# Performance work log

Hardware: AMD Instinct MI355X
Metric: run time of the kernel (lower is better)

The kernel has to match this reference:

```python
import jax, jax.numpy as jnp
import numpy as np

B, TQ, TKV, NPR, H, D = 4, 1024, 1024, 5, 16, 64
IN, OUT, R, P, NT = 1024, H * D, 64, 4096, 4
KV = NPR + TKV  # prompt tokens prepended to kv sequence


def setup_inputs() -> dict:
    key = jax.random.key(0)
    ks = jax.random.split(key, 20)
    n = lambda k, shp, s: jax.random.normal(k, shp, jnp.float32) * s
    W = 0.02  # weight init scale
    return {
        "pe": n(ks[0], (P, OUT), 1.0),
        "attn_output": n(ks[1], (B, TQ, OUT), 1.0),
        "q": n(ks[2], (B, H, TQ, D), 1.0),
        "kv_query": n(ks[3], (B, TKV, IN), 1.0),
        "attn_mask": jnp.zeros((TQ, KV), jnp.float32),
        "prompt": n(ks[4], (NT, NPR, IN), 1.0),
        "gates": n(ks[5], (1,), 1.0),
        "k_w1": n(ks[6], (IN, R), W), "k_w2": n(ks[7], (R, OUT), W),
        "v_w1": n(ks[8], (IN, R), W), "v_w2": n(ks[9], (R, OUT), W),
        "kp_w1": n(ks[10], (OUT, R), W), "kp_w2": n(ks[11], (R, OUT), W),
        "qp_w1": n(ks[12], (OUT, R), W), "qp_w2": n(ks[13], (R, OUT), W),
        "indices_a": jax.random.randint(ks[14], (B, TQ), 0, P),
        "indices_b": jax.random.randint(ks[15], (B, TKV), 0, P),
        "task_idx": jax.random.randint(ks[16], (B,), 0, NT),
    }


def reference(pe, attn_output, q, kv_query, attn_mask, prompt, gates,
              k_w1, k_w2, v_w1, v_w2, kp_w1, kp_w2, qp_w1, qp_w2,
              indices_a, indices_b, task_idx):
    # prompt selection + concat in front of kv sequence
    pr = prompt[task_idx]                                   # [B, NPR, IN]
    kv_x = jnp.concatenate([pr, kv_query], axis=1)          # [B, KV, IN]
    # positional features; key_pos is zero-padded over the prompt slots
    key_pos = jnp.pad(pe[indices_b], ((0, 0), (NPR, 0), (0, 0)))  # [B, KV, OUT]
    # low-rank projections
    k = (kv_x @ k_w1) @ k_w2 + (key_pos @ kp_w1) @ kp_w2    # [B, KV, OUT]
    v = (kv_x @ v_w1) @ v_w2                                # [B, KV, OUT]
    q_pos = (pe[indices_a] @ qp_w1) @ qp_w2                 # [B, TQ, OUT]
    qh = q + q_pos.reshape(B, TQ, H, D).transpose(0, 2, 1, 3)
    kh = k.reshape(B, KV, H, D).transpose(0, 2, 1, 3)
    vh = v.reshape(B, KV, H, D).transpose(0, 2, 1, 3)
    scores = jnp.einsum('bhqd,bhkd->bhqk', qh, kh) / np.float32(np.sqrt(D))
    scores = scores + attn_mask[None, None]                 # 2D mask path
    w = jax.nn.softmax(scores, axis=-1)                     # dropout = identity (eval)
    out = jnp.einsum('bhqk,bhkd->bhqd', w, vh)
    out = out.transpose(0, 2, 1, 3).reshape(B, TQ, OUT)
    return out * gates + attn_output
```

## Files before the change

kernel.cpp:

```cpp
#include <hip/hip_runtime.h>
#include <hip/hip_bf16.h>

#define B_    4
#define TQ_   1024
#define TKV_  1024
#define NPR_  5
#define H_    16
#define D_    64
#define IN_   1024
#define OUT_  1024
#define R_    64
#define KV_   1029
#define KVP_  1088
#define M1_   4116
#define M1P_  4160
#define MQ_   4096
#define NKT_  17
#define NQT_  16
#define MR_   (M1P_ * R_)
#define LOG2E_ 1.4426950408889634f
#define SQ_SCALE_ (0.125f * 1.4426950408889634f)

typedef __attribute__((ext_vector_type(8))) short short8;
typedef __attribute__((ext_vector_type(4))) float f32x4;
typedef __attribute__((ext_vector_type(4))) unsigned uint4v;
typedef __attribute__((ext_vector_type(2))) unsigned uint2v;

#define MFMA(a, b, c) __builtin_amdgcn_mfma_f32_16x16x32_bf16(a, b, c, 0, 0, 0)

#define AS1 __attribute__((address_space(1)))
#define AS3 __attribute__((address_space(3)))
#define GLDS(g, l) __builtin_amdgcn_global_load_lds((const AS1 void*)(g), (AS3 void*)(l), 16, 0, 0)

static __device__ __forceinline__ short f2bf(float f) {
  unsigned u = __builtin_bit_cast(unsigned, f);
  u += 0x7fffu + ((u >> 16) & 1u);
  return (short)(u >> 16);
}
static __device__ __forceinline__ float bf2f(unsigned short u) {
  return __builtin_bit_cast(float, (unsigned)u << 16);
}
static __device__ __forceinline__ short8 zero8() {
  short8 z = {0, 0, 0, 0, 0, 0, 0, 0};
  return z;
}
static __device__ __forceinline__ unsigned cvtpk(float lo, float hi) {
  unsigned r;
  asm("v_cvt_pk_bf16_f32 %0, %1, %2" : "=v"(r) : "v"(lo), "v"(hi));
  return r;
}
static __device__ __forceinline__ float vexp2(float x) {
  float r;
  asm("v_exp_f32 %0, %1" : "=v"(r) : "v"(x));
  return r;
}
static __device__ __forceinline__ void pl32(unsigned &a, unsigned &b) {
  asm("v_permlane32_swap_b32 %0, %1" : "+v"(a), "+v"(b));
}
static __device__ __forceinline__ void pl16(unsigned &a, unsigned &b) {
  asm("v_permlane16_swap_b32 %0, %1" : "+v"(a), "+v"(b));
}
static __device__ __forceinline__ float redsum4(float x) {
  unsigned a = __builtin_bit_cast(unsigned, x), b = a;
  pl16(a, b);
  x = __builtin_bit_cast(float, a) + __builtin_bit_cast(float, b);
  a = b = __builtin_bit_cast(unsigned, x);
  pl32(a, b);
  return __builtin_bit_cast(float, a) + __builtin_bit_cast(float, b);
}
static __device__ __forceinline__ void cd2bfrag(const f32x4 (&s)[4], short8 &p0, short8 &p1) {
  unsigned u00 = cvtpk(s[0][0], s[0][1]), u01 = cvtpk(s[0][2], s[0][3]);
  unsigned u10 = cvtpk(s[1][0], s[1][1]), u11 = cvtpk(s[1][2], s[1][3]);
  unsigned u20 = cvtpk(s[2][0], s[2][1]), u21 = cvtpk(s[2][2], s[2][3]);
  unsigned u30 = cvtpk(s[3][0], s[3][1]), u31 = cvtpk(s[3][2], s[3][3]);
  pl32(u00, u10); pl32(u01, u11); pl32(u20, u30); pl32(u21, u31);
  pl16(u00, u10); pl16(u01, u11); pl16(u20, u30); pl16(u21, u31);
  uint4v w0 = {u00, u01, u10, u11};
  uint4v w1 = {u20, u21, u30, u31};
  p0 = __builtin_bit_cast(short8, w0);
  p1 = __builtin_bit_cast(short8, w1);
}
static __device__ __forceinline__ short8 sum4pack(const unsigned short* p) {
  f32x4 lo = {0, 0, 0, 0}, hi = {0, 0, 0, 0};
#pragma unroll
  for (int c = 0; c < 4; ++c) {
    short8 v = *(const short8*)(p + (size_t)c * MR_);
#pragma unroll
    for (int j = 0; j < 4; ++j) {
      lo[j] += bf2f((unsigned short)v[j]);
      hi[j] += bf2f((unsigned short)v[j + 4]);
    }
  }
  uint4v u = {cvtpk(lo[0], lo[1]), cvtpk(lo[2], lo[3]),
              cvtpk(hi[0], hi[1]), cvtpk(hi[2], hi[3])};
  return __builtin_bit_cast(short8, u);
}

__global__ __launch_bounds__(256) void prep(
    const float* __restrict__ kw1, const float* __restrict__ vw1,
    const float* __restrict__ kpw1, const float* __restrict__ qpw1,
    const float* __restrict__ kw2, const float* __restrict__ vw2,
    const float* __restrict__ kpw2, const float* __restrict__ qpw2,
    const float* __restrict__ mask, const float* __restrict__ pe,
    short* __restrict__ w1t, short* __restrict__ w2t,
    short* __restrict__ pebf, int* __restrict__ mflags) {
  int bid = blockIdx.x;
  if (bid < 64) {
    int tid = bid * 256 + threadIdx.x;
    const float* w1s[4] = {kw1, vw1, kpw1, qpw1};
    const float* w2s[4] = {kw2, vw2, kpw2, qpw2};
    for (int i = tid; i < 4 * R_ * IN_; i += 64 * 256) {
      int m = i >> 16, p = i & 65535, r = p >> 10, k = p & 1023;
      w1t[i] = f2bf(w1s[m][k * R_ + r]);
    }
    for (int i = tid; i < 4 * OUT_ * R_; i += 64 * 256) {
      int m = i >> 16, p = i & 65535, o = p >> 6, r = p & 63;
      w2t[i] = f2bf(w2s[m][r * OUT_ + o]);
    }
  } else if (bid < 336) {
    int t = bid - 64;
    int qt = t / NKT_, kt = t % NKT_;
    int nz = 0;
    for (int it = 0; it < 16; ++it) {
      int e = it * 256 + threadIdx.x;
      int rr = e >> 6, cc = e & 63;
      int kv = kt * 64 + cc;
      if (kv < KV_) {
        float v = mask[(size_t)(qt * 64 + rr) * KV_ + kv];
        nz |= (v != 0.0f);
      }
    }
    __shared__ int snz[4];
    unsigned long long bv = __ballot(nz);
    if ((threadIdx.x & 63) == 0) snz[threadIdx.x >> 6] = (bv != 0ULL);
    __syncthreads();
    if (threadIdx.x == 0) mflags[t] = snz[0] | snz[1] | snz[2] | snz[3];
  } else {
    int pb = bid - 336;
#pragma unroll
    for (int it = 0; it < 8; ++it) {
      int i = pb * 16384 + it * 2048 + threadIdx.x * 8;
      f32x4 a0 = *(const f32x4*)(pe + i);
      f32x4 a1 = *(const f32x4*)(pe + i + 4);
      uint4v u = {cvtpk(a0[0], a0[1]), cvtpk(a0[2], a0[3]),
                  cvtpk(a1[0], a1[1]), cvtpk(a1[2], a1[3])};
      *(uint4v*)(pebf + i) = u;
    }
  }
}

__global__ __launch_bounds__(256) void stage1(
    const float* __restrict__ prompt, const float* __restrict__ kv_query,
    const short* __restrict__ pebf, const int* __restrict__ indices_a,
    const int* __restrict__ indices_b, const int* __restrict__ task_idx,
    const short* __restrict__ w1t, unsigned short* __restrict__ part) {
  int which = blockIdx.z;
  int chunk = blockIdx.y;
  int mbase = blockIdx.x * 64;
  int lane = threadIdx.x & 63, wave = threadIdx.x >> 6;
  int lrow = lane & 15, lg = lane >> 4;
  int row = mbase + wave * 16 + lrow;

  const float* asrc_f = nullptr;
  const short* asrc_b = nullptr;
  if (which == 0) {
    int r = min(row, M1_ - 1);
    int b = r / KV_, t = r - b * KV_;
    asrc_f = (t < NPR_) ? prompt + (size_t)(task_idx[b] * NPR_ + t) * IN_
                        : kv_query + (size_t)(b * TKV_ + t - NPR_) * IN_;
  } else if (which == 1) {
    int r = min(row, M1_ - 1);
    int b = r / KV_, t = r - b * KV_;
    if (t >= NPR_) asrc_b = pebf + (size_t)indices_b[b * TKV_ + t - NPR_] * OUT_;
  } else {
    int r = min(row, MQ_ - 1);
    asrc_b = pebf + (size_t)indices_a[r] * OUT_;
  }
  const short* bt0 = w1t + (size_t)((which == 0) ? 0 : (which == 1) ? 2 : 3) * (R_ * IN_);
  const short* bt1 = w1t + (size_t)1 * (R_ * IN_);
  int k0base = chunk * 256;

  const f32x4 fz = {0, 0, 0, 0};
  f32x4 acc0[4], acc1[4];
#pragma unroll
  for (int f = 0; f < 4; ++f) { acc0[f] = fz; acc1[f] = fz; }

#pragma unroll
  for (int ks = 0; ks < 8; ++ks) {
    int kc = k0base + ks * 32 + lg * 8;
    short8 bdat;
    if (which == 0) {
      f32x4 a0 = *(const f32x4*)(asrc_f + kc);
      f32x4 a1 = *(const f32x4*)(asrc_f + kc + 4);
      uint4v au = {cvtpk(a0[0], a0[1]), cvtpk(a0[2], a0[3]),
                   cvtpk(a1[0], a1[1]), cvtpk(a1[2], a1[3])};
      bdat = __builtin_bit_cast(short8, au);
    } else {
      bdat = asrc_b ? *(const short8*)(asrc_b + kc) : zero8();
    }
#pragma unroll
    for (int f = 0; f < 4; ++f) {
      short8 w0 = *(const short8*)(bt0 + (size_t)(f * 16 + lrow) * IN_ + kc);
      acc0[f] = MFMA(w0, bdat, acc0[f]);
      if (which == 0) {
        short8 w1f = *(const short8*)(bt1 + (size_t)(f * 16 + lrow) * IN_ + kc);
        acc1[f] = MFMA(w1f, bdat, acc1[f]);
      }
    }
  }
  int o0 = (which == 0) ? 0 : (which == 1) ? 2 : 3;
  size_t mrow = (size_t)(mbase + wave * 16 + lrow) * R_;
  unsigned short* p0 = part + (size_t)(o0 * 4 + chunk) * MR_ + mrow;
#pragma unroll
  for (int f = 0; f < 4; ++f) {
    uint2v w = {cvtpk(acc0[f][0], acc0[f][1]), cvtpk(acc0[f][2], acc0[f][3])};
    *(uint2v*)(p0 + f * 16 + lg * 4) = w;
  }
  if (which == 0) {
    unsigned short* p1 = part + (size_t)(4 + chunk) * MR_ + mrow;
#pragma unroll
    for (int f = 0; f < 4; ++f) {
      uint2v w = {cvtpk(acc1[f][0], acc1[f][1]), cvtpk(acc1[f][2], acc1[f][3])};
      *(uint2v*)(p1 + f * 16 + lg * 4) = w;
    }
  }
}

__global__ __launch_bounds__(256) void stage2(
    const unsigned short* __restrict__ part, const short* __restrict__ w2t,
    short* __restrict__ kbf, short* __restrict__ vtb, short* __restrict__ tqs) {
  int L = blockIdx.x;
  int lane = threadIdx.x & 63, wave = threadIdx.x >> 6;
  int lrow = lane & 15, lg = lane >> 4;
  const f32x4 fz = {0, 0, 0, 0};

  if (L < 272) {
    int virt = (L & 7) * 34 + (L >> 3);
    int mt = virt >> 2, nh = virt & 3;
    int orow = mt * 64 + wave * 16 + lrow;
    int ob = orow / KVP_, okv = orow - ob * KVP_;
    bool valid = (okv < KV_);
    int kt = okv >> 6, rin = okv & 63;
    int prow = ob * KV_ + min(okv, KV_ - 1);
    short8 b1[2], b2[2];
#pragma unroll
    for (int ks = 0; ks < 2; ++ks) {
      int kc = ks * 32 + lg * 8;
      b1[ks] = valid ? sum4pack(part + (size_t)prow * R_ + kc) : zero8();
      b2[ks] = valid ? sum4pack(part + (size_t)8 * MR_ + (size_t)prow * R_ + kc) : zero8();
    }
    const short* w2k  = w2t;
    const short* w2kp = w2t + (size_t)2 * (OUT_ * R_);
    int sw = (rin & 7) << 3;
#pragma unroll
    for (int i = 0; i < 4; ++i) {
      int nbase = (nh * 4 + i) * 64;
      int h = nbase >> 6;
      f32x4 acc[4];
#pragma unroll
      for (int f = 0; f < 4; ++f) acc[f] = fz;
#pragma unroll
      for (int ks = 0; ks < 2; ++ks) {
        int kc = ks * 32 + lg * 8;
#pragma unroll
        for (int f = 0; f < 4; ++f) {
          short8 aK  = *(const short8*)(w2k  + (size_t)(nbase + f * 16 + lrow) * R_ + kc);
          short8 aKP = *(const short8*)(w2kp + (size_t)(nbase + f * 16 + lrow) * R_ + kc);
          acc[f] = MFMA(aK,  b1[ks], acc[f]);
          acc[f] = MFMA(aKP, b2[ks], acc[f]);
        }
      }
      size_t tb = ((size_t)((ob * H_ + h) * NKT_ + kt) << 12);
#pragma unroll
      for (int f = 0; f < 4; ++f) {
        float v0 = valid ? acc[f][0] : 0.f, v1 = valid ? acc[f][1] : 0.f;
        float v2 = valid ? acc[f][2] : 0.f, v3 = valid ? acc[f][3] : 0.f;
        uint2v w = {cvtpk(v0, v1), cvtpk(v2, v3)};
        int d0 = f * 16 + lg * 4;
        *(uint2v*)(kbf + tb + rin * 64 + (d0 ^ sw)) = w;
      }
    }
  } else if (L < 544) {
    int Lm = L - 272;
    int virt = (Lm & 7) * 34 + (Lm >> 3);
    int cb = virt >> 2, oh = virt & 3;
    short8 afr[8];
#pragma unroll
    for (int f = 0; f < 4; ++f)
#pragma unroll
      for (int ks = 0; ks < 2; ++ks) {
        int crow = cb * 64 + f * 16 + lrow;
        int bb = crow / KVP_, kvr = crow - bb * KVP_;
        afr[f * 2 + ks] = (kvr < KV_)
            ? sum4pack(part + (size_t)4 * MR_ + (size_t)(bb * KV_ + kvr) * R_ + ks * 32 + lg * 8)
            : zero8();
      }
    int bb = (cb * 64) / KVP_;
    int kvbase = cb * 64 - bb * KVP_;
    int kt = kvbase >> 6;
    const short* w2v = w2t + (size_t)1 * (OUT_ * R_);
#pragma unroll
    for (int i = 0; i < 4; ++i) {
      int obase = (oh * 4 + i) * 64;
      int o = obase + wave * 16 + lrow;
      int h = o >> 6, d = o & 63;
      f32x4 acc[4];
#pragma unroll
      for (int f = 0; f < 4; ++f) acc[f] = fz;
#pragma unroll
      for (int ks = 0; ks < 2; ++ks) {
        short8 bw = *(const short8*)(w2v + (size_t)o * R_ + ks * 32 + lg * 8);
#pragma unroll
        for (int f = 0; f < 4; ++f) acc[f] = MFMA(afr[f * 2 + ks], bw, acc[f]);
      }
      int sw = (d & 7) << 3;
      size_t tb = ((size_t)((bb * H_ + h) * NKT_ + kt) << 12);
#pragma unroll
      for (int f = 0; f < 4; ++f) {
        int kvin0 = f * 16 + lg * 4;
        float v0 = (kvbase + kvin0 + 0 < KV_) ? acc[f][0] : 0.f;
        float v1 = (kvbase + kvin0 + 1 < KV_) ? acc[f][1] : 0.f;
        float v2 = (kvbase + kvin0 + 2 < KV_) ? acc[f][2] : 0.f;
        float v3 = (kvbase + kvin0 + 3 < KV_) ? acc[f][3] : 0.f;
        uint2v w = {cvtpk(v0, v1), cvtpk(v2, v3)};
        *(uint2v*)(vtb + tb + d * 64 + (kvin0 ^ sw)) = w;
      }
    }
  } else {
    int j = L - 544;
#pragma unroll
    for (int it = 0; it < 8; ++it) {
      int idx = j * 16384 + it * 2048 + threadIdx.x * 8;
      short8 v = sum4pack(part + (size_t)12 * MR_ + idx);
      *(short8*)(tqs + idx) = v;
    }
  }
}

__global__ __launch_bounds__(256, 3) void attn(
    const short* __restrict__ tqs, const short* __restrict__ w2t,
    const float* __restrict__ qin,
    const short* __restrict__ kbf, const short* __restrict__ vtb,
    const float* __restrict__ mask, const int* __restrict__ mflags,
    const float* __restrict__ gates, const float* __restrict__ attn_in,
    float* __restrict__ out) {
  int bid = blockIdx.x;
  int xcd = bid & 7, wg = bid >> 3;
  int qt = wg & 15, g = wg >> 4;
  int grp = xcd * 8 + g;
  int h = grp & 15, b = grp >> 4;

  int lane = threadIdx.x & 63, wave = threadIdx.x >> 6;
  int lrow = lane & 15, lg = lane >> 4;
  int qbase = qt * 64 + wave * 16;

  __shared__ __align__(16) short kvls[3][2][4096];

  const short* ktile = kbf + ((size_t)grp * NKT_ << 12);
  const short* vtile = vtb + ((size_t)grp * NKT_ << 12);
  const short* kg = ktile + wave * 512 + lane * 8;
  const short* vg = vtile + wave * 512 + lane * 8;

  int sw = (lrow & 7) << 3;
  int offA = (lg * 8) ^ sw;
  int offB = (32 + lg * 8) ^ sw;
  const short* p0A = &kvls[0][0][lrow * 64 + offA];
  const short* p0B = &kvls[0][0][lrow * 64 + offB];
  const short* p1A = &kvls[1][0][lrow * 64 + offA];
  const short* p1B = &kvls[1][0][lrow * 64 + offB];
  const short* p2A = &kvls[2][0][lrow * 64 + offA];
  const short* p2B = &kvls[2][0][lrow * 64 + offB];
  const int* mfp = mflags + qt * NKT_;

  auto stage = [&](int t, int bsel) {
    const short* ks = kg + ((size_t)t << 12);
    const short* vs = vg + ((size_t)t << 12);
    GLDS(ks,        &kvls[bsel][0][wave * 512]);
    GLDS(ks + 2048, &kvls[bsel][0][wave * 512 + 2048]);
    GLDS(vs,        &kvls[bsel][1][wave * 512]);
    GLDS(vs + 2048, &kvls[bsel][1][wave * 512 + 2048]);
  };

  stage(0, 0);
  stage(1, 1);

  int fl = 0;
#pragma unroll
  for (int t = 0; t < NKT_; ++t) fl |= (mfp[t] ? 1 : 0) << t;
  fl = __builtin_amdgcn_readfirstlane(fl);

  const f32x4 fz = {0, 0, 0, 0};
  short8 qa0, qa1;
  {
    const short* w2q = w2t + (size_t)3 * (OUT_ * R_);
    f32x4 qs[4];
#pragma unroll
    for (int f = 0; f < 4; ++f) qs[f] = fz;
#pragma unroll
    for (int ks = 0; ks < 2; ++ks) {
      short8 tqf = *(const short8*)(tqs + (size_t)(b * TQ_ + qbase + lrow) * R_ + ks * 32 + lg * 8);
#pragma unroll
      for (int f = 0; f < 4; ++f) {
        short8 wf = *(const short8*)(w2q + (size_t)(h * 64 + f * 16 + lrow) * R_ + ks * 32 + lg * 8);
        qs[f] = MFMA(wf, tqf, qs[f]);
      }
    }
    const float* qrow = qin + (size_t)(b * TQ_ + qbase + lrow) * OUT_ + h * 64;
#pragma unroll
    for (int f = 0; f < 4; ++f) {
      f32x4 qv = *(const f32x4*)(qrow + f * 16 + lg * 4);
#pragma unroll
      for (int r = 0; r < 4; ++r) qs[f][r] = (qs[f][r] + qv[r]) * SQ_SCALE_;
    }
    cd2bfrag(qs, qa0, qa1);
  }

  f32x4 oacc[4];
#pragma unroll
  for (int f = 0; f < 4; ++f) oacc[f] = fz;
  float plsum = 0.f;

  auto tile = [&](int t, const short* pA, const short* pB, int sb, int mode) {
    if (mode == 2) asm volatile("s_waitcnt vmcnt(0)" ::: "memory");
    else           asm volatile("s_waitcnt vmcnt(4)" ::: "memory");
    __builtin_amdgcn_sched_barrier(0);
    __builtin_amdgcn_s_barrier();
    __builtin_amdgcn_sched_barrier(0);
    if (mode == 0) stage(t + 2, sb);

    f32x4 s[4];
#pragma unroll
    for (int f = 0; f < 4; ++f) {
      short8 kA = *(const short8*)(pA + f * 1024);
      short8 kB = *(const short8*)(pB + f * 1024);
      s[f] = MFMA(kA, qa0, fz);
      s[f] = MFMA(kB, qa1, s[f]);
    }
    short8 vfr[8];
#pragma unroll
    for (int f = 0; f < 4; ++f) {
      vfr[f * 2 + 0] = *(const short8*)(pA + 4096 + f * 1024);
      vfr[f * 2 + 1] = *(const short8*)(pB + 4096 + f * 1024);
    }
    if ((fl >> t) & 1) {
      int kvb = t * 64;
      const float* mrp = mask + (size_t)(qbase + lrow) * KV_;
#pragma unroll
      for (int f = 0; f < 4; ++f)
#pragma unroll
        for (int r = 0; r < 4; ++r) {
          int kv = kvb + f * 16 + lg * 4 + r;
          if (kv < KV_) s[f][r] += mrp[kv] * LOG2E_;
        }
    }
    if (mode == 2) {
#pragma unroll
      for (int f = 0; f < 4; ++f)
#pragma unroll
        for (int r = 0; r < 4; ++r) {
          int kv = t * 64 + f * 16 + lg * 4 + r;
          if (kv >= KV_) s[f][r] = -1e30f;
        }
    }
#pragma unroll
    for (int f = 0; f < 4; ++f)
#pragma unroll
      for (int r = 0; r < 4; ++r) s[f][r] = vexp2(s[f][r]);
    f32x4 st = (s[0] + s[1]) + (s[2] + s[3]);
    plsum += (st[0] + st[1]) + (st[2] + st[3]);
    short8 pb0, pb1;
    cd2bfrag(s, pb0, pb1);
#pragma unroll
    for (int f = 0; f < 4; ++f) {
      oacc[f] = MFMA(vfr[f * 2 + 0], pb0, oacc[f]);
      oacc[f] = MFMA(vfr[f * 2 + 1], pb1, oacc[f]);
    }
  };

#pragma unroll 1
  for (int i = 0; i < 5; ++i) {
    tile(3 * i + 0, p0A, p0B, 2, 0);
    tile(3 * i + 1, p1A, p1B, 0, 0);
    tile(3 * i + 2, p2A, p2B, 1, 0);
  }
  tile(15, p0A, p0B, 2, 1);
  tile(16, p1A, p1B, 0, 2);

  float lsum = redsum4(plsum);
  float sc = gates[0] / lsum;
  const float* ain = attn_in + (size_t)(b * TQ_ + qbase + lrow) * OUT_ + h * 64;
  float* op = out + (size_t)(b * TQ_ + qbase + lrow) * OUT_ + h * 64;
#pragma unroll
  for (int f = 0; f < 4; ++f) {
    f32x4 av = *(const f32x4*)(ain + f * 16 + lg * 4);
    f32x4 ov;
#pragma unroll
    for (int r = 0; r < 4; ++r) ov[r] = oacc[f][r] * sc + av[r];
    *(f32x4*)(op + f * 16 + lg * 4) = ov;
  }
}

extern "C" void kernel_launch(void* const* d_in, const int* in_sizes, int n_in,
                              void* d_out, int out_size, void* d_ws, size_t ws_size,
                              hipStream_t stream) {
  const float* pe          = (const float*)d_in[0];
  const float* attn_output = (const float*)d_in[1];
  const float* q           = (const float*)d_in[2];
  const float* kv_query    = (const float*)d_in[3];
  const float* attn_mask   = (const float*)d_in[4];
  const float* prompt      = (const float*)d_in[5];
  const float* gates       = (const float*)d_in[6];
  const float* k_w1        = (const float*)d_in[7];
  const float* k_w2        = (const float*)d_in[8];
  const float* v_w1        = (const float*)d_in[9];
  const float* v_w2        = (const float*)d_in[10];
  const float* kp_w1       = (const float*)d_in[11];
  const float* kp_w2       = (const float*)d_in[12];
  const float* qp_w1       = (const float*)d_in[13];
  const float* qp_w2       = (const float*)d_in[14];
  const int* indices_a     = (const int*)d_in[15];
  const int* indices_b     = (const int*)d_in[16];
  const int* task_idx      = (const int*)d_in[17];
  float* out = (float*)d_out;

  const size_t TILEB = (size_t)64 * NKT_ * 4096;

  short* ws   = (short*)d_ws;
  short* w1t  = ws;
  short* w2t  = w1t + 4 * 65536;
  unsigned short* part = (unsigned short*)(w2t + 4 * 65536);
  short* tqs  = (short*)(part + (size_t)16 * MR_);
  int* mflags = (int*)(tqs + (size_t)MQ_ * R_);
  short* pebf = (short*)mflags + 1024;
  short* kbf  = pebf;
  short* vtb  = kbf + TILEB;

  hipLaunchKernelGGL(prep, dim3(592), dim3(256), 0, stream,
                     k_w1, v_w1, kp_w1, qp_w1, k_w2, v_w2, kp_w2, qp_w2,
                     attn_mask, pe, w1t, w2t, pebf, mflags);
  hipLaunchKernelGGL(stage1, dim3(65, 4, 3), dim3(256), 0, stream,
                     prompt, kv_query, pebf, indices_a, indices_b, task_idx, w1t, part);
  hipLaunchKernelGGL(stage2, dim3(560), dim3(256), 0, stream,
                     part, w2t, kbf, vtb, tqs);
  hipLaunchKernelGGL(attn, dim3(1024), dim3(256), 0, stream,
                     tqs, w2t, q, kbf, vtb, attn_mask, mflags, gates, attn_output, out);
}
```

Baseline: 106.5 us.

## Share K/V tiles across 8 waves per block and deepen LDS pipeline to four stages

The attention kernel now launches 512-thread blocks, each covering 128 query rows instead of 64. Each K/V tile staged into LDS is therefore reused by twice as many waves, and each wave issues half as many global-to-LDS loads. The ring buffer grows from three to four stages, with prefetch three tiles ahead and adjusted vmcnt waits, so more loads are in flight. In exchange the kernel uses more LDS per block, has fewer blocks in the grid, and runs under tighter register bounds, which may reduce occupancy or cause spills.

```diff
diff --git a/kernel.cpp b/kernel.cpp
--- a/kernel.cpp
+++ b/kernel.cpp
@@ -337,7 +337,7 @@
   }
 }
 
-__global__ __launch_bounds__(256, 3) void attn(
+__global__ __launch_bounds__(512, 4) void attn(
     const short* __restrict__ tqs, const short* __restrict__ w2t,
     const float* __restrict__ qin,
     const short* __restrict__ kbf, const short* __restrict__ vtb,
@@ -345,16 +345,17 @@
     const float* __restrict__ gates, const float* __restrict__ attn_in,
     float* __restrict__ out) {
   int bid = blockIdx.x;
-  int xcd = bid & 7, wg = bid >> 3;
-  int qt = wg & 15, g = wg >> 4;
-  int grp = xcd * 8 + g;
+  int xcd = bid & 7, rest = bid >> 3;
+  int qsup = rest & 7, gi = rest >> 3;
+  int grp = xcd * 8 + gi;
   int h = grp & 15, b = grp >> 4;
 
   int lane = threadIdx.x & 63, wave = threadIdx.x >> 6;
   int lrow = lane & 15, lg = lane >> 4;
-  int qbase = qt * 64 + wave * 16;
-
-  __shared__ __align__(16) short kvls[3][2][4096];
+  int qbase = qsup * 128 + wave * 16;
+  int qt = qsup * 2 + (wave >> 2);
+
+  __shared__ __align__(16) short kvls[4][2][4096];
 
   const short* ktile = kbf + ((size_t)grp * NKT_ << 12);
   const short* vtile = vtb + ((size_t)grp * NKT_ << 12);
@@ -364,25 +365,20 @@
   int sw = (lrow & 7) << 3;
   int offA = (lg * 8) ^ sw;
   int offB = (32 + lg * 8) ^ sw;
-  const short* p0A = &kvls[0][0][lrow * 64 + offA];
-  const short* p0B = &kvls[0][0][lrow * 64 + offB];
-  const short* p1A = &kvls[1][0][lrow * 64 + offA];
-  const short* p1B = &kvls[1][0][lrow * 64 + offB];
-  const short* p2A = &kvls[2][0][lrow * 64 + offA];
-  const short* p2B = &kvls[2][0][lrow * 64 + offB];
+  const short* pA[4] = {&kvls[0][0][lrow * 64 + offA], &kvls[1][0][lrow * 64 + offA],
+                        &kvls[2][0][lrow * 64 + offA], &kvls[3][0][lrow * 64 + offA]};
+  const short* pB[4] = {&kvls[0][0][lrow * 64 + offB], &kvls[1][0][lrow * 64 + offB],
+                        &kvls[2][0][lrow * 64 + offB], &kvls[3][0][lrow * 64 + offB]};
   const int* mfp = mflags + qt * NKT_;
 
   auto stage = [&](int t, int bsel) {
-    const short* ks = kg + ((size_t)t << 12);
-    const short* vs = vg + ((size_t)t << 12);
-    GLDS(ks,        &kvls[bsel][0][wave * 512]);
-    GLDS(ks + 2048, &kvls[bsel][0][wave * 512 + 2048]);
-    GLDS(vs,        &kvls[bsel][1][wave * 512]);
-    GLDS(vs + 2048, &kvls[bsel][1][wave * 512 + 2048]);
+    GLDS(kg + ((size_t)t << 12), &kvls[bsel][0][wave * 512]);
+    GLDS(vg + ((size_t)t << 12), &kvls[bsel][1][wave * 512]);
   };
 
   stage(0, 0);
   stage(1, 1);
+  stage(2, 2);
 
   int fl = 0;
 #pragma unroll
@@ -420,27 +416,28 @@
   for (int f = 0; f < 4; ++f) oacc[f] = fz;
   float plsum = 0.f;
 
-  auto tile = [&](int t, const short* pA, const short* pB, int sb, int mode) {
-    if (mode == 2) asm volatile("s_waitcnt vmcnt(0)" ::: "memory");
-    else           asm volatile("s_waitcnt vmcnt(4)" ::: "memory");
+  auto tile = [&](int t, const short* pa, const short* pb, int sb, int mode) {
+    if (mode == 3)      asm volatile("s_waitcnt vmcnt(0)" ::: "memory");
+    else if (mode == 2) asm volatile("s_waitcnt vmcnt(2)" ::: "memory");
+    else                asm volatile("s_waitcnt vmcnt(4)" ::: "memory");
     __builtin_amdgcn_sched_barrier(0);
     __builtin_amdgcn_s_barrier();
     __builtin_amdgcn_sched_barrier(0);
-    if (mode == 0) stage(t + 2, sb);
+    if (mode == 0) stage(t + 3, sb);
 
     f32x4 s[4];
 #pragma unroll
     for (int f = 0; f < 4; ++f) {
-      short8 kA = *(const short8*)(pA + f * 1024);
-      short8 kB = *(const short8*)(pB + f * 1024);
+      short8 kA = *(const short8*)(pa + f * 1024);
+      short8 kB = *(const short8*)(pb + f * 1024);
       s[f] = MFMA(kA, qa0, fz);
       s[f] = MFMA(kB, qa1, s[f]);
     }
     short8 vfr[8];
 #pragma unroll
     for (int f = 0; f < 4; ++f) {
-      vfr[f * 2 + 0] = *(const short8*)(pA + 4096 + f * 1024);
-      vfr[f * 2 + 1] = *(const short8*)(pB + 4096 + f * 1024);
+      vfr[f * 2 + 0] = *(const short8*)(pa + 8192 + f * 1024);
+      vfr[f * 2 + 1] = *(const short8*)(pb + 8192 + f * 1024);
     }
     if ((fl >> t) & 1) {
       int kvb = t * 64;
@@ -453,7 +450,7 @@
           if (kv < KV_) s[f][r] += mrp[kv] * LOG2E_;
         }
     }
-    if (mode == 2) {
+    if (mode == 3) {
 #pragma unroll
       for (int f = 0; f < 4; ++f)
 #pragma unroll
@@ -478,13 +475,17 @@
   };
 
 #pragma unroll 1
-  for (int i = 0; i < 5; ++i) {
-    tile(3 * i + 0, p0A, p0B, 2, 0);
-    tile(3 * i + 1, p1A, p1B, 0, 0);
-    tile(3 * i + 2, p2A, p2B, 1, 0);
-  }
-  tile(15, p0A, p0B, 2, 1);
-  tile(16, p1A, p1B, 0, 2);
+  for (int i = 0; i < 3; ++i) {
+    tile(4 * i + 0, pA[0], pB[0], 3, 0);
+    tile(4 * i + 1, pA[1], pB[1], 0, 0);
+    tile(4 * i + 2, pA[2], pB[2], 1, 0);
+    tile(4 * i + 3, pA[3], pB[3], 2, 0);
+  }
+  tile(12, pA[0], pB[0], 3, 0);
+  tile(13, pA[1], pB[1], 0, 0);
+  tile(14, pA[2], pB[2], 0, 1);
+  tile(15, pA[3], pB[3], 0, 2);
+  tile(16, pA[0], pB[0], 0, 3);
 
   float lsum = redsum4(plsum);
   float sc = gates[0] / lsum;
@@ -542,6 +543,6 @@
                      prompt, kv_query, pebf, indices_a, indices_b, task_idx, w1t, part);
   hipLaunchKernelGGL(stage2, dim3(560), dim3(256), 0, stream,
                      part, w2t, kbf, vtb, tqs);
-  hipLaunchKernelGGL(attn, dim3(1024), dim3(256), 0, stream,
+  hipLaunchKernelGGL(attn, dim3(512), dim3(512), 0, stream,
                      tqs, w2t, q, kbf, vtb, attn_mask, mflags, gates, attn_output, out);
 }
```

Measured after the change: 115.1 us. +8.0%, slower.

## Process two query sub-tiles per wave in attention to reuse K/V fragments

Applied to the files above, without the earlier changes.

Each wave of the attention kernel now handles 32 query rows as two 16-row sub-tiles, so every K and V fragment read from LDS feeds two MFMAs. The grid is halved from 1024 to 512 blocks, and each block covers 128 queries instead of 64. This cuts LDS reads and global K/V staging per query, at the cost of more registers (two score sets and two accumulators) and fewer blocks to hide latency. The mask-flag index qt is now computed per wave pair, which changes how the mask-tile flags are looked up.

```diff
diff --git a/kernel.cpp b/kernel.cpp
--- a/kernel.cpp
+++ b/kernel.cpp
@@ -345,14 +345,15 @@
     const float* __restrict__ gates, const float* __restrict__ attn_in,
     float* __restrict__ out) {
   int bid = blockIdx.x;
-  int xcd = bid & 7, wg = bid >> 3;
-  int qt = wg & 15, g = wg >> 4;
-  int grp = xcd * 8 + g;
+  int xcd = bid & 7, rest = bid >> 3;
+  int qsup = rest & 7, gi = rest >> 3;
+  int grp = xcd * 8 + gi;
   int h = grp & 15, b = grp >> 4;
 
   int lane = threadIdx.x & 63, wave = threadIdx.x >> 6;
   int lrow = lane & 15, lg = lane >> 4;
-  int qbase = qt * 64 + wave * 16;
+  int qb = qsup * 128 + wave * 32;
+  int qt = qsup * 2 + (wave >> 1);
 
   __shared__ __align__(16) short kvls[3][2][4096];
 
@@ -390,35 +391,36 @@
   fl = __builtin_amdgcn_readfirstlane(fl);
 
   const f32x4 fz = {0, 0, 0, 0};
-  short8 qa0, qa1;
-  {
+  short8 qa0[2], qa1[2];
+#pragma unroll
+  for (int p = 0; p < 2; ++p) {
     const short* w2q = w2t + (size_t)3 * (OUT_ * R_);
     f32x4 qs[4];
 #pragma unroll
     for (int f = 0; f < 4; ++f) qs[f] = fz;
 #pragma unroll
     for (int ks = 0; ks < 2; ++ks) {
-      short8 tqf = *(const short8*)(tqs + (size_t)(b * TQ_ + qbase + lrow) * R_ + ks * 32 + lg * 8);
+      short8 tqf = *(const short8*)(tqs + (size_t)(b * TQ_ + qb + p * 16 + lrow) * R_ + ks * 32 + lg * 8);
 #pragma unroll
       for (int f = 0; f < 4; ++f) {
         short8 wf = *(const short8*)(w2q + (size_t)(h * 64 + f * 16 + lrow) * R_ + ks * 32 + lg * 8);
         qs[f] = MFMA(wf, tqf, qs[f]);
       }
     }
-    const float* qrow = qin + (size_t)(b * TQ_ + qbase + lrow) * OUT_ + h * 64;
+    const float* qrow = qin + (size_t)(b * TQ_ + qb + p * 16 + lrow) * OUT_ + h * 64;
 #pragma unroll
     for (int f = 0; f < 4; ++f) {
       f32x4 qv = *(const f32x4*)(qrow + f * 16 + lg * 4);
 #pragma unroll
       for (int r = 0; r < 4; ++r) qs[f][r] = (qs[f][r] + qv[r]) * SQ_SCALE_;
     }
-    cd2bfrag(qs, qa0, qa1);
-  }
-
-  f32x4 oacc[4];
-#pragma unroll
-  for (int f = 0; f < 4; ++f) oacc[f] = fz;
-  float plsum = 0.f;
+    cd2bfrag(qs, qa0[p], qa1[p]);
+  }
+
+  f32x4 oa0[4], oa1[4];
+#pragma unroll
+  for (int f = 0; f < 4; ++f) { oa0[f] = fz; oa1[f] = fz; }
+  float plsum0 = 0.f, plsum1 = 0.f;
 
   auto tile = [&](int t, const short* pA, const short* pB, int sb, int mode) {
     if (mode == 2) asm volatile("s_waitcnt vmcnt(0)" ::: "memory");
@@ -428,29 +430,29 @@
     __builtin_amdgcn_sched_barrier(0);
     if (mode == 0) stage(t + 2, sb);
 
-    f32x4 s[4];
+    f32x4 s0[4], s1[4];
 #pragma unroll
     for (int f = 0; f < 4; ++f) {
       short8 kA = *(const short8*)(pA + f * 1024);
       short8 kB = *(const short8*)(pB + f * 1024);
-      s[f] = MFMA(kA, qa0, fz);
-      s[f] = MFMA(kB, qa1, s[f]);
-    }
-    short8 vfr[8];
-#pragma unroll
-    for (int f = 0; f < 4; ++f) {
-      vfr[f * 2 + 0] = *(const short8*)(pA + 4096 + f * 1024);
-      vfr[f * 2 + 1] = *(const short8*)(pB + 4096 + f * 1024);
+      s0[f] = MFMA(kA, qa0[0], fz);
+      s0[f] = MFMA(kB, qa1[0], s0[f]);
+      s1[f] = MFMA(kA, qa0[1], fz);
+      s1[f] = MFMA(kB, qa1[1], s1[f]);
     }
     if ((fl >> t) & 1) {
       int kvb = t * 64;
-      const float* mrp = mask + (size_t)(qbase + lrow) * KV_;
+      const float* mrp0 = mask + (size_t)(qb + lrow) * KV_;
+      const float* mrp1 = mask + (size_t)(qb + 16 + lrow) * KV_;
 #pragma unroll
       for (int f = 0; f < 4; ++f)
 #pragma unroll
         for (int r = 0; r < 4; ++r) {
           int kv = kvb + f * 16 + lg * 4 + r;
-          if (kv < KV_) s[f][r] += mrp[kv] * LOG2E_;
+          if (kv < KV_) {
+            s0[f][r] += mrp0[kv] * LOG2E_;
+            s1[f][r] += mrp1[kv] * LOG2E_;
+          }
         }
     }
     if (mode == 2) {
@@ -459,21 +461,31 @@
 #pragma unroll
         for (int r = 0; r < 4; ++r) {
           int kv = t * 64 + f * 16 + lg * 4 + r;
-          if (kv >= KV_) s[f][r] = -1e30f;
+          if (kv >= KV_) { s0[f][r] = -1e30f; s1[f][r] = -1e30f; }
         }
     }
 #pragma unroll
     for (int f = 0; f < 4; ++f)
 #pragma unroll
-      for (int r = 0; r < 4; ++r) s[f][r] = vexp2(s[f][r]);
-    f32x4 st = (s[0] + s[1]) + (s[2] + s[3]);
-    plsum += (st[0] + st[1]) + (st[2] + st[3]);
-    short8 pb0, pb1;
-    cd2bfrag(s, pb0, pb1);
+      for (int r = 0; r < 4; ++r) {
+        s0[f][r] = vexp2(s0[f][r]);
+        s1[f][r] = vexp2(s1[f][r]);
+      }
+    f32x4 st0 = (s0[0] + s0[1]) + (s0[2] + s0[3]);
+    f32x4 st1 = (s1[0] + s1[1]) + (s1[2] + s1[3]);
+    plsum0 += (st0[0] + st0[1]) + (st0[2] + st0[3]);
+    plsum1 += (st1[0] + st1[1]) + (st1[2] + st1[3]);
+    short8 pbA0, pbA1, pbB0, pbB1;
+    cd2bfrag(s0, pbA0, pbA1);
+    cd2bfrag(s1, pbB0, pbB1);
 #pragma unroll
     for (int f = 0; f < 4; ++f) {
-      oacc[f] = MFMA(vfr[f * 2 + 0], pb0, oacc[f]);
-      oacc[f] = MFMA(vfr[f * 2 + 1], pb1, oacc[f]);
+      short8 vA = *(const short8*)(pA + 4096 + f * 1024);
+      short8 vB = *(const short8*)(pB + 4096 + f * 1024);
+      oa0[f] = MFMA(vA, pbA0, oa0[f]);
+      oa0[f] = MFMA(vB, pbA1, oa0[f]);
+      oa1[f] = MFMA(vA, pbB0, oa1[f]);
+      oa1[f] = MFMA(vB, pbB1, oa1[f]);
     }
   };
 
@@ -486,17 +498,24 @@
   tile(15, p0A, p0B, 2, 1);
   tile(16, p1A, p1B, 0, 2);
 
-  float lsum = redsum4(plsum);
-  float sc = gates[0] / lsum;
-  const float* ain = attn_in + (size_t)(b * TQ_ + qbase + lrow) * OUT_ + h * 64;
-  float* op = out + (size_t)(b * TQ_ + qbase + lrow) * OUT_ + h * 64;
-#pragma unroll
-  for (int f = 0; f < 4; ++f) {
-    f32x4 av = *(const f32x4*)(ain + f * 16 + lg * 4);
-    f32x4 ov;
-#pragma unroll
-    for (int r = 0; r < 4; ++r) ov[r] = oacc[f][r] * sc + av[r];
-    *(f32x4*)(op + f * 16 + lg * 4) = ov;
+  float lsum0 = redsum4(plsum0);
+  float lsum1 = redsum4(plsum1);
+  float g = gates[0];
+  float sc0 = g / lsum0, sc1 = g / lsum1;
+#pragma unroll
+  for (int p = 0; p < 2; ++p) {
+    float sc = p ? sc1 : sc0;
+    const f32x4* oa = p ? oa1 : oa0;
+    const float* ain = attn_in + (size_t)(b * TQ_ + qb + p * 16 + lrow) * OUT_ + h * 64;
+    float* op = out + (size_t)(b * TQ_ + qb + p * 16 + lrow) * OUT_ + h * 64;
+#pragma unroll
+    for (int f = 0; f < 4; ++f) {
+      f32x4 av = *(const f32x4*)(ain + f * 16 + lg * 4);
+      f32x4 ov;
+#pragma unroll
+      for (int r = 0; r < 4; ++r) ov[r] = oa[f][r] * sc + av[r];
+      *(f32x4*)(op + f * 16 + lg * 4) = ov;
+    }
   }
 }
 
@@ -542,6 +561,6 @@
                      prompt, kv_query, pebf, indices_a, indices_b, task_idx, w1t, part);
   hipLaunchKernelGGL(stage2, dim3(560), dim3(256), 0, stream,
                      part, w2t, kbf, vtb, tqs);
-  hipLaunchKernelGGL(attn, dim3(1024), dim3(256), 0, stream,
+  hipLaunchKernelGGL(attn, dim3(512), dim3(256), 0, stream,
                      tqs, w2t, q, kbf, vtb, attn_mask, mflags, gates, attn_output, out);
 }
```

Result: slower. 109.3 us (+2.6%).
